# Performance work log

Measured on AMD Instinct MI355X. Metric: run time of the kernel, lower is better.

## Reference

```python
import jax, jax.numpy as jnp
import numpy as np

B, C, L, E = 65536, 16, 32, 32
EPS = 1e-12

def _normalize(x, axis=-1):
    # F.normalize: x / max(||x||_2, eps)
    n = jnp.sqrt(jnp.sum(x * x, axis=axis, keepdims=True))
    return x / jnp.maximum(n, EPS)

def _linear(x, W, b):
    # torch nn.Linear: y = x @ W.T + b, W: [out, in]
    return jnp.einsum('bcl,el->bce', x, W) + b

def setup_inputs() -> dict:
    key = jax.random.key(0)
    ks = jax.random.split(key, 12)
    s_l = 1.0 / np.sqrt(L)
    s_p1 = 1.0 / np.sqrt(C * E)
    s_p2 = 1.0 / np.sqrt(C * 3)
    return {
        'embed1': jax.random.normal(ks[0], (B, C, L), jnp.float32),
        'embed2': jax.random.normal(ks[1], (B, C, L), jnp.float32),
        'qW': jax.random.uniform(ks[2], (E, L), jnp.float32, -s_l, s_l),
        'qb': jax.random.uniform(ks[3], (E,), jnp.float32, -s_l, s_l),
        'kW': jax.random.uniform(ks[4], (E, L), jnp.float32, -s_l, s_l),
        'kb': jax.random.uniform(ks[5], (E,), jnp.float32, -s_l, s_l),
        'vW': jax.random.uniform(ks[6], (E, L), jnp.float32, -s_l, s_l),
        'vb': jax.random.uniform(ks[7], (E,), jnp.float32, -s_l, s_l),
        'p1W': jax.random.uniform(ks[8], (C * 3, C * E), jnp.float32, -s_p1, s_p1),
        'p1b': jax.random.uniform(ks[9], (C * 3,), jnp.float32, -s_p1, s_p1),
        'p2W': jax.random.uniform(ks[10], (3, C * 3), jnp.float32, -s_p2, s_p2),
        'p2b': jax.random.uniform(ks[11], (3,), jnp.float32, -s_p2, s_p2),
    }

def reference(embed1, embed2, qW, qb, kW, kb, vW, vb, p1W, p1b, p2W, p2b):
    query = _linear(embed1, qW, qb) * _linear(embed2, qW, qb)   # [B,C,E]
    key_t = _linear(embed1, kW, kb) * _linear(embed2, kW, kb)   # [B,C,E]
    value = _linear(embed1, vW, vb) * _linear(embed2, vW, vb)   # [B,C,E]
    attn = jnp.einsum('bce,bde->bcd', _normalize(query), _normalize(key_t))  # [B,C,C]
    # torch F.softmax with dim=None on a 3-D tensor -> legacy dim=0 (batch axis)
    attn = jax.nn.softmax(attn, axis=0)
    # dropout(p=0.2) is identity in eval mode
    out = jnp.einsum('bcd,bce->bde', attn, value)  # attn.transpose(1,2) @ value, [B,C,E]
    h = out.reshape(out.shape[0], -1)              # [B, C*E]
    h = jax.nn.relu(h @ p1W.T + p1b) @ p2W.T + p2b  # [B, 3]
    return _normalize(h)
```

## Files before the change

### kernel.cpp

```cpp
#include <hip/hip_runtime.h>

#define B_TOT 65536
#define WS_P1W 4096
#define WS_EV  (1u << 20)
#define EV_BYTES 100663296u
#define WS_PART (WS_EV + EV_BYTES)

typedef float f32x4 __attribute__((ext_vector_type(4)));
typedef short s16x8 __attribute__((ext_vector_type(8)));

__device__ __forceinline__ float bf2f(unsigned short h) {
    unsigned u = ((unsigned)h) << 16;
    return __builtin_bit_cast(float, u);
}
__device__ __forceinline__ unsigned pack2(float a, float b) {
    unsigned ua = __builtin_bit_cast(unsigned, a) + 0x8000u;
    unsigned ub = __builtin_bit_cast(unsigned, b) + 0x8000u;
    return __builtin_amdgcn_perm(ub, ua, 0x07060302u);
}
__device__ __forceinline__ unsigned short f2bf(float f) {
    return (unsigned short)((__builtin_bit_cast(unsigned, f) + 0x8000u) >> 16);
}
__device__ __forceinline__ s16x8 cvt8(float4 a, float4 b) {
    uint4 u;
    u.x = pack2(a.x, a.y); u.y = pack2(a.z, a.w);
    u.z = pack2(b.x, b.y); u.w = pack2(b.z, b.w);
    return __builtin_bit_cast(s16x8, u);
}
#define MFMA(a, b, c) __builtin_amdgcn_mfma_f32_16x16x32_bf16((a), (b), (c), 0, 0, 0)

__global__ __launch_bounds__(256) void k1_stats(
    const float* __restrict__ e1, const float* __restrict__ e2,
    const float* __restrict__ qW, const float* __restrict__ qb,
    const float* __restrict__ kW, const float* __restrict__ kb,
    const float* __restrict__ vW, const float* __restrict__ vb,
    char* __restrict__ ws) {

    const int tid = threadIdx.x;
    const int lane = tid & 63;
    const int widx = tid >> 6;
    const int col = lane & 15;
    const int quad = lane >> 4;

    __shared__ __align__(16) unsigned short qk_lds[4][2][16 * 40];
    __shared__ float Dblk[256];
    Dblk[tid] = 0.f;
    __syncthreads();

    s16x8 wq[2], wk[2], wv[2];
    f32x4 cbq[2], cbk[2], cbv[2];
#pragma unroll
    for (int h = 0; h < 2; ++h) {
        int row = col + 16 * h;
        const float4* pq = (const float4*)(qW + row * 32 + quad * 8);
        const float4* pk = (const float4*)(kW + row * 32 + quad * 8);
        const float4* pv = (const float4*)(vW + row * 32 + quad * 8);
        wq[h] = cvt8(pq[0], pq[1]);
        wk[h] = cvt8(pk[0], pk[1]);
        wv[h] = cvt8(pv[0], pv[1]);
        float qv_ = qb[row], kv_ = kb[row], vv_ = vb[row];
        cbq[h] = (f32x4){qv_, qv_, qv_, qv_};
        cbk[h] = (f32x4){kv_, kv_, kv_, kv_};
        cbv[h] = (f32x4){vv_, vv_, vv_, vv_};
    }

    unsigned short* qbuf = qk_lds[widx][0];
    unsigned short* kbuf = qk_lds[widx][1];
    float dacc[4] = {0.f, 0.f, 0.f, 0.f};
    char* evbase = ws + WS_EV;
    const f32x4 z = {0.f, 0.f, 0.f, 0.f};

    const int gw = blockIdx.x * 4 + widx;
    for (int i = 0; i < 8; ++i) {
        const int b = gw * 8 + i;
        const float4* x1p = (const float4*)(e1 + (size_t)b * 512 + col * 32 + quad * 8);
        const float4* x2p = (const float4*)(e2 + (size_t)b * 512 + col * 32 + quad * 8);
        float4 a0 = x1p[0], a1 = x1p[1];
        float4 b0 = x2p[0], b1 = x2p[1];
        s16x8 fx1 = cvt8(a0, a1);
        s16x8 fx2 = cvt8(b0, b1);

        {
            f32x4 q1v[2], q2v[2];
#pragma unroll
            for (int h = 0; h < 2; ++h) {
                q1v[h] = MFMA(fx1, wq[h], cbq[h]);
                q2v[h] = MFMA(fx2, wq[h], cbq[h]);
            }
#pragma unroll
            for (int r = 0; r < 4; ++r) {
                int w = (quad * 4 + r) * 20 + col;
                ((unsigned*)qbuf)[w] = pack2(q1v[0][r] * q2v[0][r],
                                             q1v[1][r] * q2v[1][r]);
            }
        }
        {
            f32x4 k1v[2], k2v[2];
#pragma unroll
            for (int h = 0; h < 2; ++h) {
                k1v[h] = MFMA(fx1, wk[h], cbk[h]);
                k2v[h] = MFMA(fx2, wk[h], cbk[h]);
            }
#pragma unroll
            for (int r = 0; r < 4; ++r) {
                int w = (quad * 4 + r) * 20 + col;
                ((unsigned*)kbuf)[w] = pack2(k1v[0][r] * k2v[0][r],
                                             k1v[1][r] * k2v[1][r]);
            }
        }
        char* bbase = evbase + (size_t)b * 1536;
        {
            f32x4 v1v[2], v2v[2];
#pragma unroll
            for (int h = 0; h < 2; ++h) {
                v1v[h] = MFMA(fx1, wv[h], cbv[h]);
                v2v[h] = MFMA(fx2, wv[h], cbv[h]);
            }
#pragma unroll
            for (int h = 0; h < 2; ++h) {
                uint2 vst;
                vst.x = pack2(v1v[h][0] * v2v[h][0], v1v[h][1] * v2v[h][1]);
                vst.y = pack2(v1v[h][2] * v2v[h][2], v1v[h][3] * v2v[h][3]);
                *(uint2*)(bbase + 512 + ((h * 16 + col) * 2 + (quad >> 1)) * 16 + (quad & 1) * 8) = vst;
            }
        }

        s16x8 aq  = *(const s16x8*)(qbuf + col * 40 + quad * 8);
        s16x8 bk8 = *(const s16x8*)(kbuf + col * 40 + quad * 8);
        f32x4 S = MFMA(aq, bk8, z);

        float ssq = 0.f, ssk = 0.f;
#pragma unroll
        for (int j = 0; j < 8; ++j) {
            float qf = bf2f((unsigned short)aq[j]);  ssq += qf * qf;
            float kf = bf2f((unsigned short)bk8[j]); ssk += kf * kf;
        }
        ssq += __shfl_xor(ssq, 16); ssq += __shfl_xor(ssq, 32);
        ssk += __shfl_xor(ssk, 16); ssk += __shfl_xor(ssk, 32);
        float invq = 1.f / fmaxf(sqrtf(ssq), 1e-12f);
        float invk = 1.f / fmaxf(sqrtf(ssk), 1e-12f);
        float iq0 = __shfl(invq, quad * 4 + 0);
        float iq1 = __shfl(invq, quad * 4 + 1);
        float iq2 = __shfl(invq, quad * 4 + 2);
        float iq3 = __shfl(invq, quad * 4 + 3);

        float ex0 = __expf(S[0] * (iq0 * invk));
        float ex1 = __expf(S[1] * (iq1 * invk));
        float ex2 = __expf(S[2] * (iq2 * invk));
        float ex3 = __expf(S[3] * (iq3 * invk));
        dacc[0] += ex0; dacc[1] += ex1; dacc[2] += ex2; dacc[3] += ex3;
        uint2 est; est.x = pack2(ex0, ex1); est.y = pack2(ex2, ex3);
        *(uint2*)(bbase + col * 32 + quad * 8) = est;
    }
#pragma unroll
    for (int r = 0; r < 4; ++r)
        atomicAdd(&Dblk[col * 16 + quad * 4 + r], dacc[r]);
    __syncthreads();
    ((float*)(ws + WS_PART))[blockIdx.x * 256 + tid] = Dblk[tid];
}

__global__ __launch_bounds__(256) void k1b_prep(const float* __restrict__ p1W,
                                                char* __restrict__ ws) {
    const int t = threadIdx.x;
    const int idx = blockIdx.x * 256 + t;
    if (idx < 24576) {
        int jj   = idx & 7;
        int lane = (idx >> 3) & 63;
        int ktnt = idx >> 9;
        int kt = ktnt & 15, nt = ktnt >> 4;
        int n_lo = lane & 15, q8 = lane >> 4;
        int j2  = nt * 16 + n_lo;
        int ip  = kt * 32 + q8 * 8 + jj;
        int e_lo = ip >> 5, qq = (ip >> 3) & 3, hh = (ip >> 2) & 1, r = ip & 3;
        int orig = (qq * 4 + r) * 32 + (e_lo + 16 * hh);
        ((unsigned short*)(ws + WS_P1W))[idx] = f2bf(p1W[j2 * 512 + orig]);
    }
    const float* part = (const float*)(ws + WS_PART);
    const int j = blockIdx.x;
    float s = 0.f;
#pragma unroll
    for (int k = 0; k < 8; ++k)
        s += part[(size_t)(k * 256 + t) * 256 + j];
    __shared__ float red[256];
    red[t] = s;
    __syncthreads();
    for (int o = 128; o > 0; o >>= 1) {
        if (t < o) red[t] += red[t + o];
        __syncthreads();
    }
    if (t == 0) ((float*)ws)[j] = 1.f / red[0];
}

__global__ __launch_bounds__(256) void k2_apply(
    const char* __restrict__ ws, const float* __restrict__ p1b,
    const float* __restrict__ p2W, const float* __restrict__ p2b,
    float* __restrict__ out) {

    const int tid = threadIdx.x;
    const int lane = tid & 63;
    const int widx = tid >> 6;
    const int col = lane & 15;
    const int quad = lane >> 4;
    const int qm = quad & 1;

    __shared__ __align__(16) unsigned short Hs[16 * 512];
    float* P = (float*)Hs;

    float p1bias[3], p2w[3][3];
#pragma unroll
    for (int nt = 0; nt < 3; ++nt) {
        p1bias[nt] = p1b[col + 16 * nt];
#pragma unroll
        for (int t2 = 0; t2 < 3; ++t2) p2w[nt][t2] = p2W[t2 * 48 + col + 16 * nt];
    }
    const float pb0 = p2b[0], pb1 = p2b[1], pb2 = p2b[2];

    const float* Dws = (const float*)ws;
    const float4 dva = *(const float4*)(Dws + col * 16 + qm * 8);
    const float4 dvb = *(const float4*)(Dws + col * 16 + qm * 8 + 4);
    float dinv[8] = {dva.x, dva.y, dva.z, dva.w, dvb.x, dvb.y, dvb.z, dvb.w};

    const char* evbase = ws + WS_EV;
    const unsigned short* p1wp = (const unsigned short*)(ws + WS_P1W);
    const int g = blockIdx.x;
    const f32x4 z = {0.f, 0.f, 0.f, 0.f};
    const s16x8 zz = {0, 0, 0, 0, 0, 0, 0, 0};

    {
        const char* bb0 = evbase + (size_t)(g * 16 + widx * 4) * 1536;
        const int eoff  = col * 32 + qm * 16;
        const int voff0 = 512 + (col * 2 + qm) * 16;
        const int voff1 = 512 + ((16 + col) * 2 + qm) * 16;
        s16x8 ne  = *(const s16x8*)(bb0 + eoff);
        s16x8 nv0 = *(const s16x8*)(bb0 + voff0);
        s16x8 nv1 = *(const s16x8*)(bb0 + voff1);
#pragma unroll
        for (int ii = 0; ii < 4; ++ii) {
            s16x8 eraw = ne, bf0 = nv0, bf1 = nv1;
            if (ii < 3) {
                const char* nb = bb0 + (size_t)(ii + 1) * 1536;
                ne  = *(const s16x8*)(nb + eoff);
                nv0 = *(const s16x8*)(nb + voff0);
                nv1 = *(const s16x8*)(nb + voff1);
            }
            float ef[8];
#pragma unroll
            for (int j = 0; j < 8; ++j)
                ef[j] = bf2f((unsigned short)eraw[j]) * dinv[j];
            uint4 ua;
            ua.x = pack2(ef[0], ef[1]); ua.y = pack2(ef[2], ef[3]);
            ua.z = pack2(ef[4], ef[5]); ua.w = pack2(ef[6], ef[7]);
            s16x8 afrag = __builtin_bit_cast(s16x8, ua);
            if (quad >= 2) { afrag = zz; bf0 = zz; bf1 = zz; }
            f32x4 o0 = MFMA(afrag, bf0, z);
            f32x4 o1 = MFMA(afrag, bf1, z);
            uint4 uh;
            uh.x = pack2(o0[0], o0[1]); uh.y = pack2(o0[2], o0[3]);
            uh.z = pack2(o1[0], o1[1]); uh.w = pack2(o1[2], o1[3]);
            const int i = widx * 4 + ii;
            int chunk = (col * 4 + quad) ^ (i & 7);
            *(uint4*)(Hs + i * 512 + chunk * 8) = uh;
        }
    }
    __syncthreads();

    f32x4 acc[3] = {z, z, z};
    {
        const int kt0 = widx * 4;
        s16x8 nw0 = *(const s16x8*)(p1wp + ((0 * 16 + kt0) * 64 + lane) * 8);
        s16x8 nw1 = *(const s16x8*)(p1wp + ((1 * 16 + kt0) * 64 + lane) * 8);
        s16x8 nw2 = *(const s16x8*)(p1wp + ((2 * 16 + kt0) * 64 + lane) * 8);
#pragma unroll
        for (int t2 = 0; t2 < 4; ++t2) {
            const int kt = widx * 4 + t2;
            s16x8 w0 = nw0, w1 = nw1, w2 = nw2;
            if (t2 < 3) {
                nw0 = *(const s16x8*)(p1wp + ((0 * 16 + kt + 1) * 64 + lane) * 8);
                nw1 = *(const s16x8*)(p1wp + ((1 * 16 + kt + 1) * 64 + lane) * 8);
                nw2 = *(const s16x8*)(p1wp + ((2 * 16 + kt + 1) * 64 + lane) * 8);
            }
            int chunk = (kt * 4 + quad) ^ (col & 7);
            s16x8 a = *(const s16x8*)(Hs + col * 512 + chunk * 8);
            acc[0] = MFMA(a, w0, acc[0]);
            acc[1] = MFMA(a, w1, acc[1]);
            acc[2] = MFMA(a, w2, acc[2]);
        }
    }
    __syncthreads();

#pragma unroll
    for (int nt = 0; nt < 3; ++nt)
        *(f32x4*)(P + (widx * 64 + lane) * 12 + nt * 4) = acc[nt];
    __syncthreads();

    {
        float s3[3] = {0.f, 0.f, 0.f};
#pragma unroll
        for (int w = 0; w < 4; ++w)
#pragma unroll
            for (int nt = 0; nt < 3; ++nt)
                s3[nt] += P[(w * 64 + lane) * 12 + nt * 4 + widx];
        float pp[3] = {0.f, 0.f, 0.f};
#pragma unroll
        for (int nt = 0; nt < 3; ++nt) {
            float hv = fmaxf(s3[nt] + p1bias[nt], 0.f);
            pp[0] += hv * p2w[nt][0];
            pp[1] += hv * p2w[nt][1];
            pp[2] += hv * p2w[nt][2];
        }
#pragma unroll
        for (int m = 1; m <= 8; m <<= 1) {
            pp[0] += __shfl_xor(pp[0], m);
            pp[1] += __shfl_xor(pp[1], m);
            pp[2] += __shfl_xor(pp[2], m);
        }
        float h0 = pp[0] + pb0, h1 = pp[1] + pb1, h2 = pp[2] + pb2;
        float inv = 1.f / fmaxf(sqrtf(h0 * h0 + h1 * h1 + h2 * h2), 1e-12f);
        if (col < 3) {
            float v = (col == 0) ? h0 : ((col == 1) ? h1 : h2);
            out[(size_t)(g * 16 + quad * 4 + widx) * 3 + col] = v * inv;
        }
    }
}

extern "C" void kernel_launch(void* const* d_in, const int* in_sizes, int n_in,
                              void* d_out, int out_size, void* d_ws, size_t ws_size,
                              hipStream_t stream) {
    const float* e1  = (const float*)d_in[0];
    const float* e2  = (const float*)d_in[1];
    const float* qW  = (const float*)d_in[2];
    const float* qb  = (const float*)d_in[3];
    const float* kW  = (const float*)d_in[4];
    const float* kb  = (const float*)d_in[5];
    const float* vW  = (const float*)d_in[6];
    const float* vb  = (const float*)d_in[7];
    const float* p1W = (const float*)d_in[8];
    const float* p1b = (const float*)d_in[9];
    const float* p2W = (const float*)d_in[10];
    const float* p2b = (const float*)d_in[11];
    float* out = (float*)d_out;
    char* ws = (char*)d_ws;

    k1_stats<<<2048, 256, 0, stream>>>(e1, e2, qW, qb, kW, kb, vW, vb, ws);
    k1b_prep<<<256, 256, 0, stream>>>(p1W, ws);
    k2_apply<<<4096, 256, 0, stream>>>(ws, p1b, p2W, p2b, out);
}
```

Measured before the change: 337.0 us.

## Interleave two batches per k1 iteration and parallelize denominator reduction with atomics

The stats kernel now loads and processes two batch elements per loop step, using double-buffered LDS tiles, so loads and MFMAs of independent samples can overlap. Biases are added after bias-free MFMAs rather than being folded into the accumulator. The kernel is launched as two half-grids with a block offset. The softmax denominator reduction is reworked: 16 blocks each sum 128 partials and atomically add into a buffer that the first k1 launch zeroes, with the reciprocal moved into k2. This adds register pressure in k1 and an extra launch, and float atomics make the summation order nondeterministic.

```diff
diff --git a/kernel.cpp b/kernel.cpp
--- a/kernel.cpp
+++ b/kernel.cpp
@@ -34,7 +34,7 @@
     const float* __restrict__ qW, const float* __restrict__ qb,
     const float* __restrict__ kW, const float* __restrict__ kb,
     const float* __restrict__ vW, const float* __restrict__ vb,
-    char* __restrict__ ws) {
+    char* __restrict__ ws, int blkoff) {
 
     const int tid = threadIdx.x;
     const int lane = tid & 63;
@@ -42,13 +42,14 @@
     const int col = lane & 15;
     const int quad = lane >> 4;
 
-    __shared__ __align__(16) unsigned short qk_lds[4][2][16 * 40];
+    __shared__ __align__(16) unsigned short qk_lds[4][2][2][16 * 40];
     __shared__ float Dblk[256];
+    if (blkoff == 0 && blockIdx.x == 0) ((float*)ws)[tid] = 0.f;
     Dblk[tid] = 0.f;
     __syncthreads();
 
     s16x8 wq[2], wk[2], wv[2];
-    f32x4 cbq[2], cbk[2], cbv[2];
+    float bq[2], bk[2], bv[2];
 #pragma unroll
     for (int h = 0; h < 2; ++h) {
         int row = col + 16 * h;
@@ -58,112 +59,113 @@
         wq[h] = cvt8(pq[0], pq[1]);
         wk[h] = cvt8(pk[0], pk[1]);
         wv[h] = cvt8(pv[0], pv[1]);
-        float qv_ = qb[row], kv_ = kb[row], vv_ = vb[row];
-        cbq[h] = (f32x4){qv_, qv_, qv_, qv_};
-        cbk[h] = (f32x4){kv_, kv_, kv_, kv_};
-        cbv[h] = (f32x4){vv_, vv_, vv_, vv_};
-    }
-
-    unsigned short* qbuf = qk_lds[widx][0];
-    unsigned short* kbuf = qk_lds[widx][1];
+        bq[h] = qb[row]; bk[h] = kb[row]; bv[h] = vb[row];
+    }
+
     float dacc[4] = {0.f, 0.f, 0.f, 0.f};
     char* evbase = ws + WS_EV;
     const f32x4 z = {0.f, 0.f, 0.f, 0.f};
 
-    const int gw = blockIdx.x * 4 + widx;
-    for (int i = 0; i < 8; ++i) {
-        const int b = gw * 8 + i;
-        const float4* x1p = (const float4*)(e1 + (size_t)b * 512 + col * 32 + quad * 8);
-        const float4* x2p = (const float4*)(e2 + (size_t)b * 512 + col * 32 + quad * 8);
-        float4 a0 = x1p[0], a1 = x1p[1];
-        float4 b0 = x2p[0], b1 = x2p[1];
-        s16x8 fx1 = cvt8(a0, a1);
-        s16x8 fx2 = cvt8(b0, b1);
-
-        {
-            f32x4 q1v[2], q2v[2];
-#pragma unroll
-            for (int h = 0; h < 2; ++h) {
-                q1v[h] = MFMA(fx1, wq[h], cbq[h]);
-                q2v[h] = MFMA(fx2, wq[h], cbq[h]);
-            }
-#pragma unroll
-            for (int r = 0; r < 4; ++r) {
-                int w = (quad * 4 + r) * 20 + col;
-                ((unsigned*)qbuf)[w] = pack2(q1v[0][r] * q2v[0][r],
-                                             q1v[1][r] * q2v[1][r]);
-            }
-        }
-        {
-            f32x4 k1v[2], k2v[2];
-#pragma unroll
-            for (int h = 0; h < 2; ++h) {
-                k1v[h] = MFMA(fx1, wk[h], cbk[h]);
-                k2v[h] = MFMA(fx2, wk[h], cbk[h]);
-            }
-#pragma unroll
-            for (int r = 0; r < 4; ++r) {
-                int w = (quad * 4 + r) * 20 + col;
-                ((unsigned*)kbuf)[w] = pack2(k1v[0][r] * k2v[0][r],
-                                             k1v[1][r] * k2v[1][r]);
-            }
-        }
-        char* bbase = evbase + (size_t)b * 1536;
-        {
-            f32x4 v1v[2], v2v[2];
-#pragma unroll
-            for (int h = 0; h < 2; ++h) {
-                v1v[h] = MFMA(fx1, wv[h], cbv[h]);
-                v2v[h] = MFMA(fx2, wv[h], cbv[h]);
-            }
-#pragma unroll
-            for (int h = 0; h < 2; ++h) {
-                uint2 vst;
-                vst.x = pack2(v1v[h][0] * v2v[h][0], v1v[h][1] * v2v[h][1]);
-                vst.y = pack2(v1v[h][2] * v2v[h][2], v1v[h][3] * v2v[h][3]);
-                *(uint2*)(bbase + 512 + ((h * 16 + col) * 2 + (quad >> 1)) * 16 + (quad & 1) * 8) = vst;
-            }
-        }
-
-        s16x8 aq  = *(const s16x8*)(qbuf + col * 40 + quad * 8);
-        s16x8 bk8 = *(const s16x8*)(kbuf + col * 40 + quad * 8);
-        f32x4 S = MFMA(aq, bk8, z);
-
-        float ssq = 0.f, ssk = 0.f;
-#pragma unroll
-        for (int j = 0; j < 8; ++j) {
-            float qf = bf2f((unsigned short)aq[j]);  ssq += qf * qf;
-            float kf = bf2f((unsigned short)bk8[j]); ssk += kf * kf;
-        }
-        ssq += __shfl_xor(ssq, 16); ssq += __shfl_xor(ssq, 32);
-        ssk += __shfl_xor(ssk, 16); ssk += __shfl_xor(ssk, 32);
-        float invq = 1.f / fmaxf(sqrtf(ssq), 1e-12f);
-        float invk = 1.f / fmaxf(sqrtf(ssk), 1e-12f);
-        float iq0 = __shfl(invq, quad * 4 + 0);
-        float iq1 = __shfl(invq, quad * 4 + 1);
-        float iq2 = __shfl(invq, quad * 4 + 2);
-        float iq3 = __shfl(invq, quad * 4 + 3);
-
-        float ex0 = __expf(S[0] * (iq0 * invk));
-        float ex1 = __expf(S[1] * (iq1 * invk));
-        float ex2 = __expf(S[2] * (iq2 * invk));
-        float ex3 = __expf(S[3] * (iq3 * invk));
-        dacc[0] += ex0; dacc[1] += ex1; dacc[2] += ex2; dacc[3] += ex3;
-        uint2 est; est.x = pack2(ex0, ex1); est.y = pack2(ex2, ex3);
-        *(uint2*)(bbase + col * 32 + quad * 8) = est;
+    const int gw = (blkoff + blockIdx.x) * 4 + widx;
+    for (int i = 0; i < 4; ++i) {
+        s16x8 fx1[2], fx2[2];
+#pragma unroll
+        for (int p = 0; p < 2; ++p) {
+            const int b = gw * 8 + i * 2 + p;
+            const float4* x1p = (const float4*)(e1 + (size_t)b * 512 + col * 32 + quad * 8);
+            const float4* x2p = (const float4*)(e2 + (size_t)b * 512 + col * 32 + quad * 8);
+            float4 a0 = x1p[0], a1 = x1p[1];
+            float4 b0 = x2p[0], b1 = x2p[1];
+            fx1[p] = cvt8(a0, a1);
+            fx2[p] = cvt8(b0, b1);
+        }
+#pragma unroll
+        for (int p = 0; p < 2; ++p) {
+            const int b = gw * 8 + i * 2 + p;
+            char* bbase = evbase + (size_t)b * 1536;
+            {
+                f32x4 qa = MFMA(fx1[p], wq[0], z), qc = MFMA(fx2[p], wq[0], z);
+                f32x4 qd = MFMA(fx1[p], wq[1], z), qe = MFMA(fx2[p], wq[1], z);
+                unsigned* dst = (unsigned*)qk_lds[widx][0][p];
+#pragma unroll
+                for (int r = 0; r < 4; ++r)
+                    dst[(quad * 4 + r) * 20 + col] =
+                        pack2((qa[r] + bq[0]) * (qc[r] + bq[0]),
+                              (qd[r] + bq[1]) * (qe[r] + bq[1]));
+            }
+            {
+                f32x4 ka = MFMA(fx1[p], wk[0], z), kc = MFMA(fx2[p], wk[0], z);
+                f32x4 kd = MFMA(fx1[p], wk[1], z), ke = MFMA(fx2[p], wk[1], z);
+                unsigned* dst = (unsigned*)qk_lds[widx][1][p];
+#pragma unroll
+                for (int r = 0; r < 4; ++r)
+                    dst[(quad * 4 + r) * 20 + col] =
+                        pack2((ka[r] + bk[0]) * (kc[r] + bk[0]),
+                              (kd[r] + bk[1]) * (ke[r] + bk[1]));
+            }
+            {
+                f32x4 va = MFMA(fx1[p], wv[0], z), vc = MFMA(fx2[p], wv[0], z);
+                f32x4 vd = MFMA(fx1[p], wv[1], z), ve = MFMA(fx2[p], wv[1], z);
+                uint2 vst0, vst1;
+                vst0.x = pack2((va[0] + bv[0]) * (vc[0] + bv[0]),
+                               (va[1] + bv[0]) * (vc[1] + bv[0]));
+                vst0.y = pack2((va[2] + bv[0]) * (vc[2] + bv[0]),
+                               (va[3] + bv[0]) * (vc[3] + bv[0]));
+                vst1.x = pack2((vd[0] + bv[1]) * (ve[0] + bv[1]),
+                               (vd[1] + bv[1]) * (ve[1] + bv[1]));
+                vst1.y = pack2((vd[2] + bv[1]) * (ve[2] + bv[1]),
+                               (vd[3] + bv[1]) * (ve[3] + bv[1]));
+                *(uint2*)(bbase + 512 + ((0 * 16 + col) * 2 + (quad >> 1)) * 16 + (quad & 1) * 8) = vst0;
+                *(uint2*)(bbase + 512 + ((1 * 16 + col) * 2 + (quad >> 1)) * 16 + (quad & 1) * 8) = vst1;
+            }
+        }
+#pragma unroll
+        for (int p = 0; p < 2; ++p) {
+            const int b = gw * 8 + i * 2 + p;
+            char* bbase = evbase + (size_t)b * 1536;
+            const unsigned short* qbuf = qk_lds[widx][0][p];
+            const unsigned short* kbuf = qk_lds[widx][1][p];
+            s16x8 aq  = *(const s16x8*)(qbuf + col * 40 + quad * 8);
+            s16x8 bk8 = *(const s16x8*)(kbuf + col * 40 + quad * 8);
+            f32x4 S = MFMA(aq, bk8, z);
+
+            float ssq = 0.f, ssk = 0.f;
+#pragma unroll
+            for (int j = 0; j < 8; ++j) {
+                float qf = bf2f((unsigned short)aq[j]);  ssq += qf * qf;
+                float kf = bf2f((unsigned short)bk8[j]); ssk += kf * kf;
+            }
+            ssq += __shfl_xor(ssq, 16); ssq += __shfl_xor(ssq, 32);
+            ssk += __shfl_xor(ssk, 16); ssk += __shfl_xor(ssk, 32);
+            float invq = 1.f / fmaxf(sqrtf(ssq), 1e-12f);
+            float invk = 1.f / fmaxf(sqrtf(ssk), 1e-12f);
+            float iq0 = __shfl(invq, quad * 4 + 0);
+            float iq1 = __shfl(invq, quad * 4 + 1);
+            float iq2 = __shfl(invq, quad * 4 + 2);
+            float iq3 = __shfl(invq, quad * 4 + 3);
+
+            float ex0 = __expf(S[0] * (iq0 * invk));
+            float ex1 = __expf(S[1] * (iq1 * invk));
+            float ex2 = __expf(S[2] * (iq2 * invk));
+            float ex3 = __expf(S[3] * (iq3 * invk));
+            dacc[0] += ex0; dacc[1] += ex1; dacc[2] += ex2; dacc[3] += ex3;
+            uint2 est; est.x = pack2(ex0, ex1); est.y = pack2(ex2, ex3);
+            *(uint2*)(bbase + col * 32 + quad * 8) = est;
+        }
     }
 #pragma unroll
     for (int r = 0; r < 4; ++r)
         atomicAdd(&Dblk[col * 16 + quad * 4 + r], dacc[r]);
     __syncthreads();
-    ((float*)(ws + WS_PART))[blockIdx.x * 256 + tid] = Dblk[tid];
+    ((float*)(ws + WS_PART))[(size_t)(blkoff + blockIdx.x) * 256 + tid] = Dblk[tid];
 }
 
 __global__ __launch_bounds__(256) void k1b_prep(const float* __restrict__ p1W,
                                                 char* __restrict__ ws) {
     const int t = threadIdx.x;
-    const int idx = blockIdx.x * 256 + t;
-    if (idx < 24576) {
+    const int g = blockIdx.x;
+    const int idx = g * 256 + t;
+    {
         int jj   = idx & 7;
         int lane = (idx >> 3) & 63;
         int ktnt = idx >> 9;
@@ -175,20 +177,13 @@
         int orig = (qq * 4 + r) * 32 + (e_lo + 16 * hh);
         ((unsigned short*)(ws + WS_P1W))[idx] = f2bf(p1W[j2 * 512 + orig]);
     }
-    const float* part = (const float*)(ws + WS_PART);
-    const int j = blockIdx.x;
-    float s = 0.f;
-#pragma unroll
-    for (int k = 0; k < 8; ++k)
-        s += part[(size_t)(k * 256 + t) * 256 + j];
-    __shared__ float red[256];
-    red[t] = s;
-    __syncthreads();
-    for (int o = 128; o > 0; o >>= 1) {
-        if (t < o) red[t] += red[t + o];
-        __syncthreads();
-    }
-    if (t == 0) ((float*)ws)[j] = 1.f / red[0];
+    if (g < 16) {
+        const float* part = (const float*)(ws + WS_PART);
+        float s = 0.f;
+        for (int r = 0; r < 128; ++r)
+            s += part[(size_t)(g * 128 + r) * 256 + t];
+        atomicAdd(((float*)ws) + t, s);
+    }
 }
 
 __global__ __launch_bounds__(256) void k2_apply(
@@ -218,7 +213,8 @@
     const float* Dws = (const float*)ws;
     const float4 dva = *(const float4*)(Dws + col * 16 + qm * 8);
     const float4 dvb = *(const float4*)(Dws + col * 16 + qm * 8 + 4);
-    float dinv[8] = {dva.x, dva.y, dva.z, dva.w, dvb.x, dvb.y, dvb.z, dvb.w};
+    float dinv[8] = {1.f / dva.x, 1.f / dva.y, 1.f / dva.z, 1.f / dva.w,
+                     1.f / dvb.x, 1.f / dvb.y, 1.f / dvb.z, 1.f / dvb.w};
 
     const char* evbase = ws + WS_EV;
     const unsigned short* p1wp = (const unsigned short*)(ws + WS_P1W);
@@ -341,7 +337,8 @@
     float* out = (float*)d_out;
     char* ws = (char*)d_ws;
 
-    k1_stats<<<2048, 256, 0, stream>>>(e1, e2, qW, qb, kW, kb, vW, vb, ws);
-    k1b_prep<<<256, 256, 0, stream>>>(p1W, ws);
+    k1_stats<<<1024, 256, 0, stream>>>(e1, e2, qW, qb, kW, kb, vW, vb, ws, 0);
+    k1_stats<<<1024, 256, 0, stream>>>(e1, e2, qW, qb, kW, kb, vW, vb, ws, 1024);
+    k1b_prep<<<96, 256, 0, stream>>>(p1W, ws);
     k2_apply<<<4096, 256, 0, stream>>>(ws, p1b, p2W, p2b, out);
 }
```

New measurement: 352.6 us. +4.6%, slower.

## Fold p1W prep and denominator reduction into stats kernel via atomics

Applied to the files above, without the earlier changes.

Drops the separate k1b_prep kernel. The p1W bf16 repack moves into the first 96 blocks of k1_stats, and the per-block softmax denominators are summed with global float atomics into a buffer zeroed by a memset. k2 now takes the reciprocal itself. The exp and value intermediates are written with nontemporal stores to reduce cache pollution. This saves one launch and the partial-sum round trip, but adds a memset, atomic contention on 256 addresses, and a non-deterministic summation order.

```diff
diff --git a/kernel.cpp b/kernel.cpp
--- a/kernel.cpp
+++ b/kernel.cpp
@@ -3,11 +3,10 @@
 #define B_TOT 65536
 #define WS_P1W 4096
 #define WS_EV  (1u << 20)
-#define EV_BYTES 100663296u
-#define WS_PART (WS_EV + EV_BYTES)
 
 typedef float f32x4 __attribute__((ext_vector_type(4)));
 typedef short s16x8 __attribute__((ext_vector_type(8)));
+typedef unsigned u32x2 __attribute__((ext_vector_type(2)));
 
 __device__ __forceinline__ float bf2f(unsigned short h) {
     unsigned u = ((unsigned)h) << 16;
@@ -34,7 +33,7 @@
     const float* __restrict__ qW, const float* __restrict__ qb,
     const float* __restrict__ kW, const float* __restrict__ kb,
     const float* __restrict__ vW, const float* __restrict__ vb,
-    char* __restrict__ ws) {
+    const float* __restrict__ p1W, char* __restrict__ ws) {
 
     const int tid = threadIdx.x;
     const int lane = tid & 63;
@@ -45,6 +44,20 @@
     __shared__ __align__(16) unsigned short qk_lds[4][2][16 * 40];
     __shared__ float Dblk[256];
     Dblk[tid] = 0.f;
+
+    if (blockIdx.x < 96) {
+        int idx = blockIdx.x * 256 + tid;
+        int jj   = idx & 7;
+        int l2   = (idx >> 3) & 63;
+        int ktnt = idx >> 9;
+        int kt = ktnt & 15, nt = ktnt >> 4;
+        int n_lo = l2 & 15, q8 = l2 >> 4;
+        int j2  = nt * 16 + n_lo;
+        int ip  = kt * 32 + q8 * 8 + jj;
+        int e_lo = ip >> 5, qq = (ip >> 3) & 3, hh = (ip >> 2) & 1, r = ip & 3;
+        int orig = (qq * 4 + r) * 32 + (e_lo + 16 * hh);
+        ((unsigned short*)(ws + WS_P1W))[idx] = f2bf(p1W[j2 * 512 + orig]);
+    }
     __syncthreads();
 
     s16x8 wq[2], wk[2], wv[2];
@@ -118,10 +131,11 @@
             }
 #pragma unroll
             for (int h = 0; h < 2; ++h) {
-                uint2 vst;
+                u32x2 vst;
                 vst.x = pack2(v1v[h][0] * v2v[h][0], v1v[h][1] * v2v[h][1]);
                 vst.y = pack2(v1v[h][2] * v2v[h][2], v1v[h][3] * v2v[h][3]);
-                *(uint2*)(bbase + 512 + ((h * 16 + col) * 2 + (quad >> 1)) * 16 + (quad & 1) * 8) = vst;
+                __builtin_nontemporal_store(vst,
+                    (u32x2*)(bbase + 512 + ((h * 16 + col) * 2 + (quad >> 1)) * 16 + (quad & 1) * 8));
             }
         }
 
@@ -149,46 +163,14 @@
         float ex2 = __expf(S[2] * (iq2 * invk));
         float ex3 = __expf(S[3] * (iq3 * invk));
         dacc[0] += ex0; dacc[1] += ex1; dacc[2] += ex2; dacc[3] += ex3;
-        uint2 est; est.x = pack2(ex0, ex1); est.y = pack2(ex2, ex3);
-        *(uint2*)(bbase + col * 32 + quad * 8) = est;
+        u32x2 est; est.x = pack2(ex0, ex1); est.y = pack2(ex2, ex3);
+        __builtin_nontemporal_store(est, (u32x2*)(bbase + col * 32 + quad * 8));
     }
 #pragma unroll
     for (int r = 0; r < 4; ++r)
         atomicAdd(&Dblk[col * 16 + quad * 4 + r], dacc[r]);
     __syncthreads();
-    ((float*)(ws + WS_PART))[blockIdx.x * 256 + tid] = Dblk[tid];
-}
-
-__global__ __launch_bounds__(256) void k1b_prep(const float* __restrict__ p1W,
-                                                char* __restrict__ ws) {
-    const int t = threadIdx.x;
-    const int idx = blockIdx.x * 256 + t;
-    if (idx < 24576) {
-        int jj   = idx & 7;
-        int lane = (idx >> 3) & 63;
-        int ktnt = idx >> 9;
-        int kt = ktnt & 15, nt = ktnt >> 4;
-        int n_lo = lane & 15, q8 = lane >> 4;
-        int j2  = nt * 16 + n_lo;
-        int ip  = kt * 32 + q8 * 8 + jj;
-        int e_lo = ip >> 5, qq = (ip >> 3) & 3, hh = (ip >> 2) & 1, r = ip & 3;
-        int orig = (qq * 4 + r) * 32 + (e_lo + 16 * hh);
-        ((unsigned short*)(ws + WS_P1W))[idx] = f2bf(p1W[j2 * 512 + orig]);
-    }
-    const float* part = (const float*)(ws + WS_PART);
-    const int j = blockIdx.x;
-    float s = 0.f;
-#pragma unroll
-    for (int k = 0; k < 8; ++k)
-        s += part[(size_t)(k * 256 + t) * 256 + j];
-    __shared__ float red[256];
-    red[t] = s;
-    __syncthreads();
-    for (int o = 128; o > 0; o >>= 1) {
-        if (t < o) red[t] += red[t + o];
-        __syncthreads();
-    }
-    if (t == 0) ((float*)ws)[j] = 1.f / red[0];
+    atomicAdd(((float*)ws) + tid, Dblk[tid]);
 }
 
 __global__ __launch_bounds__(256) void k2_apply(
@@ -218,7 +200,8 @@
     const float* Dws = (const float*)ws;
     const float4 dva = *(const float4*)(Dws + col * 16 + qm * 8);
     const float4 dvb = *(const float4*)(Dws + col * 16 + qm * 8 + 4);
-    float dinv[8] = {dva.x, dva.y, dva.z, dva.w, dvb.x, dvb.y, dvb.z, dvb.w};
+    float dinv[8] = {1.f / dva.x, 1.f / dva.y, 1.f / dva.z, 1.f / dva.w,
+                     1.f / dvb.x, 1.f / dvb.y, 1.f / dvb.z, 1.f / dvb.w};
 
     const char* evbase = ws + WS_EV;
     const unsigned short* p1wp = (const unsigned short*)(ws + WS_P1W);
@@ -341,7 +324,7 @@
     float* out = (float*)d_out;
     char* ws = (char*)d_ws;
 
-    k1_stats<<<2048, 256, 0, stream>>>(e1, e2, qW, qb, kW, kb, vW, vb, ws);
-    k1b_prep<<<256, 256, 0, stream>>>(p1W, ws);
+    (void)hipMemsetAsync(ws, 0, 1024, stream);
+    k1_stats<<<2048, 256, 0, stream>>>(e1, e2, qW, qb, kW, kb, vW, vb, p1W, ws);
     k2_apply<<<4096, 256, 0, stream>>>(ws, p1b, p2W, p2b, out);
 }
```

Result: slower. 354.0 us (+5.0%).
